# Kernel tuning notes

Hardware: AMD Instinct MI355X
Metric: run time of the kernel (lower is better)

## Reference

```python
import jax, jax.numpy as jnp
import numpy as np

D_MODEL = 1024
N_HEADS = 16
D_Q = 64
D_V = 64
N_SEG = 16
EPS_LN = 1e-5
EPS_MEM = 1e-6


def setup_inputs() -> dict:
    key = jax.random.key(0)
    ks = jax.random.split(key, 10)
    N, T = 4, 4096
    inp = {
        "query_sequences": jax.random.normal(ks[0], (N, T, D_MODEL), dtype=jnp.float32),
        "key_sequences": jax.random.normal(ks[1], (N, T, D_MODEL), dtype=jnp.float32),
        "value_sequences": jax.random.normal(ks[2], (N, T, D_MODEL), dtype=jnp.float32),
        "Wq": jax.random.normal(ks[3], (D_MODEL, N_HEADS * D_Q), dtype=jnp.float32) * 0.02,
        "Wk": jax.random.normal(ks[4], (D_MODEL, N_HEADS * D_Q), dtype=jnp.float32) * 0.02,
        "Wv": jax.random.normal(ks[5], (D_MODEL, N_HEADS * D_V), dtype=jnp.float32) * 0.02,
        "Wo": jax.random.normal(ks[6], (N_HEADS * D_V, D_MODEL), dtype=jnp.float32) * 0.02,
        "ln_w": jnp.ones((D_MODEL,), dtype=jnp.float32),
        "ln_b": jnp.zeros((D_MODEL,), dtype=jnp.float32),
        "beta": jnp.ones((1,), dtype=jnp.float32),
    }
    return inp


def _layer_norm(x, w, b):
    mu = jnp.mean(x, axis=-1, keepdims=True)
    var = jnp.var(x, axis=-1, keepdims=True)
    return (x - mu) * jax.lax.rsqrt(var + EPS_LN) * w + b


def reference(query_sequences, key_sequences, value_sequences, Wq, Wk, Wv, Wo, ln_w, ln_b, beta):
    N, t, _ = query_sequences.shape
    S = t // N_SEG  # segment length (256)

    # qkv_norm applied to q, and (self-attention) to k and v as well
    qn = _layer_norm(query_sequences, ln_w, ln_b)
    kn = _layer_norm(key_sequences, ln_w, ln_b)
    vn = _layer_norm(value_sequences, ln_w, ln_b)

    # project and split heads -> [N, H, t, d]
    qh = (qn @ Wq).reshape(N, t, N_HEADS, D_Q).transpose(0, 2, 1, 3)
    kh = (kn @ Wk).reshape(N, t, N_HEADS, D_Q).transpose(0, 2, 1, 3)
    vh = (vn @ Wv).reshape(N, t, N_HEADS, D_V).transpose(0, 2, 1, 3)

    # segment: [N_SEG, N, H, S, d] so lax.scan iterates segments sequentially
    seg = lambda x, d: x.reshape(N, N_HEADS, N_SEG, S, d).transpose(2, 0, 1, 3, 4)
    q_segs, k_segs, v_segs = seg(qh, D_Q), seg(kh, D_Q), seg(vh, D_V)

    b_gate = jax.nn.sigmoid(beta)[0]            # scalar mixing gate
    scale = 1.0 / np.sqrt(D_Q).astype(np.float32)
    causal = jnp.tril(jnp.ones((S, S), dtype=bool))

    def step(carry, xs):
        mem, z = carry                          # [N,H,Dq,Dv], [N,H,Dq]
        qs, ks_, vs = xs                        # [N,H,S,d]
        sq = jax.nn.elu(qs) + 1.0
        sk = jax.nn.elu(ks_) + 1.0
        # retrieve from compressive memory
        num = jnp.einsum('nhsd,nhde->nhse', sq, mem)
        den = jnp.einsum('nhsd,nhd->nhs', sq, z)[..., None] + EPS_MEM
        a_mem = num / den                       # [N,H,S,Dv]
        # local causal softmax attention within the segment
        scores = jnp.einsum('nhsd,nhtd->nhst', qs, ks_) * scale
        scores = jnp.where(causal, scores, -jnp.inf)
        probs = jax.nn.softmax(scores, axis=-1)
        attn = jnp.einsum('nhst,nhtd->nhsd', probs, vs)
        out = b_gate * a_mem + (1.0 - b_gate) * attn
        # linear memory update
        mem = mem + jnp.einsum('nhsd,nhse->nhde', sk, vs)
        z = z + sk.sum(axis=2)
        return (mem, z), out

    mem0 = jnp.zeros((N, N_HEADS, D_Q, D_V), dtype=query_sequences.dtype)
    z0 = jnp.zeros((N, N_HEADS, D_Q), dtype=query_sequences.dtype)
    _, outs = jax.lax.scan(step, (mem0, z0), (q_segs, k_segs, v_segs))

    # outs: [N_SEG, N, H, S, Dv] -> [N, t, H*Dv]
    seqs = outs.transpose(1, 0, 3, 2, 4).reshape(N, t, N_HEADS * D_V)
    return seqs @ Wo
```

## Files before the change

kernel.cpp:

```cpp
#include <hip/hip_runtime.h>
#include <stdint.h>
#include <math.h>


typedef __attribute__((ext_vector_type(8))) short bf16x8_t;
typedef __attribute__((ext_vector_type(4))) short short4_t;
typedef __attribute__((ext_vector_type(4))) float f32x4;

__device__ __forceinline__ float bf2f(short s){
  union { unsigned u; float f; } v; v.u = ((unsigned)(unsigned short)s) << 16; return v.f;
}
__device__ __forceinline__ short f2bf(float f){
  union { float fl; unsigned u; } v; v.fl = f;
  unsigned r = v.u + 0x7FFFu + ((v.u >> 16) & 1u);
  return (short)(unsigned short)(r >> 16);
}
__device__ __forceinline__ f32x4 mfma16(bf16x8_t a, bf16x8_t b, f32x4 c){
  return __builtin_amdgcn_mfma_f32_16x16x32_bf16(a, b, c, 0, 0, 0);
}
__device__ __forceinline__ void gl_lds16(const short* g, short* l){
  __builtin_amdgcn_global_load_lds((const __attribute__((address_space(1))) void*)g,
                                   (__attribute__((address_space(3))) void*)l, 16, 0, 0);
}

__global__ __launch_bounds__(256) void ln3(const float* __restrict__ xq, const float* __restrict__ xk,
                                           const float* __restrict__ xv,
                                           const float* __restrict__ gw, const float* __restrict__ gb,
                                           short* __restrict__ oq, short* __restrict__ ok,
                                           short* __restrict__ ov){
  const int row = blockIdx.x, which = blockIdx.y, tid = threadIdx.x;
  const float* x = which == 0 ? xq : which == 1 ? xk : xv;
  short* out     = which == 0 ? oq : which == 1 ? ok : ov;
  const float4 v = *reinterpret_cast<const float4*>(x + (size_t)row*1024 + tid*4);
  float s  = v.x + v.y + v.z + v.w;
  float s2 = v.x*v.x + v.y*v.y + v.z*v.z + v.w*v.w;
  #pragma unroll
  for (int off = 1; off < 64; off <<= 1){
    s  += __shfl_xor(s,  off);
    s2 += __shfl_xor(s2, off);
  }
  __shared__ float red[8];
  if ((tid & 63) == 0){ red[tid>>6] = s; red[4 + (tid>>6)] = s2; }
  __syncthreads();
  s  = red[0] + red[1] + red[2] + red[3];
  s2 = red[4] + red[5] + red[6] + red[7];
  const float mu  = s * (1.0f/1024.0f);
  const float var = s2 * (1.0f/1024.0f) - mu*mu;
  const float rs  = rsqrtf(var + 1e-5f);
  const float4 wv = *reinterpret_cast<const float4*>(gw + tid*4);
  const float4 bv = *reinterpret_cast<const float4*>(gb + tid*4);
  short4_t o;
  o[0] = f2bf((v.x-mu)*rs*wv.x + bv.x);
  o[1] = f2bf((v.y-mu)*rs*wv.y + bv.y);
  o[2] = f2bf((v.z-mu)*rs*wv.z + bv.z);
  o[3] = f2bf((v.w-mu)*rs*wv.w + bv.w);
  *reinterpret_cast<short4_t*>(out + (size_t)row*1024 + tid*4) = o;
}

__global__ __launch_bounds__(256) void wcast4(const float* __restrict__ W0, const float* __restrict__ W1,
                                              const float* __restrict__ W2, const float* __restrict__ W3,
                                              short* __restrict__ T0, short* __restrict__ T1,
                                              short* __restrict__ T2, short* __restrict__ T3){
  const int z = blockIdx.z;
  const float* W = z == 0 ? W0 : z == 1 ? W1 : z == 2 ? W2 : W3;
  short* Wt      = z == 0 ? T0 : z == 1 ? T1 : z == 2 ? T2 : T3;
  __shared__ float tile[64][65];
  const int bx = blockIdx.x, by = blockIdx.y, tid = threadIdx.x;
  #pragma unroll
  for (int p=0;p<4;++p){
    int idx = p*256 + tid;
    int r = idx >> 4, c4 = (idx & 15) << 2;
    const float4 v = *reinterpret_cast<const float4*>(W + (size_t)(by*64 + r)*1024 + bx*64 + c4);
    tile[r][c4+0] = v.x; tile[r][c4+1] = v.y; tile[r][c4+2] = v.z; tile[r][c4+3] = v.w;
  }
  __syncthreads();
  #pragma unroll
  for (int p=0;p<4;++p){
    int idx = p*256 + tid;
    int r = idx >> 4, c4 = (idx & 15) << 2;
    short4_t o;
    o[0] = f2bf(tile[c4+0][r]); o[1] = f2bf(tile[c4+1][r]);
    o[2] = f2bf(tile[c4+2][r]); o[3] = f2bf(tile[c4+3][r]);
    *reinterpret_cast<short4_t*>(Wt + (size_t)(bx*64 + r)*1024 + by*64 + c4) = o;
  }
}

__device__ __forceinline__ void remap_mc(int n, int& m0, int& c0){
  int xcd = n & 7, idx = n >> 3;
  m0 = ((xcd << 3) + (idx & 7)) << 8;
  c0 = (idx >> 3) << 8;
}

__device__ __forceinline__ void gemm_body(short* smem, const short* __restrict__ A,
                                          const short* __restrict__ Bt, void* __restrict__ C,
                                          int mode, int m0, int c0){
  short* As = smem;
  short* Bs = smem + 32768;
  const int tid = threadIdx.x;
  const int lane = tid & 63, wid = tid >> 6;
  const int wr = wid >> 2, wc = wid & 3;
  const int l15 = lane & 15, lhi = lane >> 4;

  const short* Asrc[4]; const short* Bsrc[4];
  #pragma unroll
  for (int p=0;p<4;++p){
    int i = tid + 512*p;
    int r = i >> 3, g = (i & 7) ^ (r & 7);
    Asrc[p] = A  + (size_t)(m0 + r)*1024 + g*8;
    Bsrc[p] = Bt + (size_t)(c0 + r)*1024 + g*8;
  }

  f32x4 acc[8][4];
  #pragma unroll
  for (int m=0;m<8;++m)
    #pragma unroll
    for (int n=0;n<4;++n) acc[m][n] = (f32x4){0.f,0.f,0.f,0.f};

  #define STAGE_A(t) { short* _d=&As[((t)&1)<<14]; int _k=(t)<<6; \
      gl_lds16(Asrc[0]+_k, _d+tid*8); gl_lds16(Asrc[1]+_k, _d+4096+tid*8); \
      gl_lds16(Asrc[2]+_k, _d+8192+tid*8); gl_lds16(Asrc[3]+_k, _d+12288+tid*8); }
  #define STAGE_B(t) { short* _d=&Bs[((t)&1)<<14]; int _k=(t)<<6; \
      gl_lds16(Bsrc[0]+_k, _d+tid*8); gl_lds16(Bsrc[1]+_k, _d+4096+tid*8); \
      gl_lds16(Bsrc[2]+_k, _d+8192+tid*8); gl_lds16(Bsrc[3]+_k, _d+12288+tid*8); }

  STAGE_A(0); STAGE_B(0);
  asm volatile("s_waitcnt vmcnt(0)" ::: "memory");
  __builtin_amdgcn_s_barrier();

  for (int t = 0; t < 16; ++t){
    const short* Ab = &As[(t & 1) << 14];
    const short* Bb = &Bs[(t & 1) << 14];
    if (t < 15){ STAGE_A(t+1); STAGE_B(t+1); }
    bf16x8_t af[4][2], bfr[4][2];
    #pragma unroll
    for (int m=0;m<4;++m){
      int r = wr*128 + m*16 + l15;
      #pragma unroll
      for (int ks=0;ks<2;++ks){
        int sl = (ks*4 + lhi) ^ (r & 7);
        af[m][ks] = *reinterpret_cast<const bf16x8_t*>(&Ab[r*64 + sl*8]);
      }
    }
    #pragma unroll
    for (int n=0;n<2;++n){
      int r = wc*64 + n*16 + l15;
      #pragma unroll
      for (int ks=0;ks<2;++ks){
        int sl = (ks*4 + lhi) ^ (r & 7);
        bfr[n][ks] = *reinterpret_cast<const bf16x8_t*>(&Bb[r*64 + sl*8]);
      }
    }
    __builtin_amdgcn_s_setprio(1);
    #pragma unroll
    for (int m=0;m<4;++m)
      #pragma unroll
      for (int n=0;n<2;++n)
        #pragma unroll
        for (int ks=0;ks<2;++ks)
          acc[m][n] = mfma16(af[m][ks], bfr[n][ks], acc[m][n]);
    __builtin_amdgcn_s_setprio(0);
    #pragma unroll
    for (int n=2;n<4;++n){
      int r = wc*64 + n*16 + l15;
      #pragma unroll
      for (int ks=0;ks<2;++ks){
        int sl = (ks*4 + lhi) ^ (r & 7);
        bfr[n][ks] = *reinterpret_cast<const bf16x8_t*>(&Bb[r*64 + sl*8]);
      }
    }
    __builtin_amdgcn_s_setprio(1);
    #pragma unroll
    for (int m=0;m<4;++m)
      #pragma unroll
      for (int n=2;n<4;++n)
        #pragma unroll
        for (int ks=0;ks<2;++ks)
          acc[m][n] = mfma16(af[m][ks], bfr[n][ks], acc[m][n]);
    __builtin_amdgcn_s_setprio(0);
    #pragma unroll
    for (int m=0;m<4;++m){
      int r = wr*128 + 64 + m*16 + l15;
      #pragma unroll
      for (int ks=0;ks<2;++ks){
        int sl = (ks*4 + lhi) ^ (r & 7);
        af[m][ks] = *reinterpret_cast<const bf16x8_t*>(&Ab[r*64 + sl*8]);
      }
    }
    __builtin_amdgcn_s_setprio(1);
    #pragma unroll
    for (int m=0;m<4;++m)
      #pragma unroll
      for (int n=0;n<2;++n)
        #pragma unroll
        for (int ks=0;ks<2;++ks)
          acc[4+m][n] = mfma16(af[m][ks], bfr[n][ks], acc[4+m][n]);
    __builtin_amdgcn_s_setprio(0);
    __builtin_amdgcn_s_setprio(1);
    #pragma unroll
    for (int m=0;m<4;++m)
      #pragma unroll
      for (int n=2;n<4;++n)
        #pragma unroll
        for (int ks=0;ks<2;++ks)
          acc[4+m][n] = mfma16(af[m][ks], bfr[n][ks], acc[4+m][n]);
    __builtin_amdgcn_s_setprio(0);
    asm volatile("s_waitcnt vmcnt(0)" ::: "memory");
    __builtin_amdgcn_s_barrier();
  }
  #undef STAGE_A
  #undef STAGE_B

  if (mode == 0){
    short* Cb = (short*)C;
    #pragma unroll
    for (int m=0;m<8;++m)
      #pragma unroll
      for (int n=0;n<4;++n)
        #pragma unroll
        for (int j=0;j<4;++j){
          int row = m0 + wr*128 + m*16 + lhi*4 + j;
          int col = c0 + wc*64 + n*16 + l15;
          size_t oidx = ((size_t)((row>>12)*16 + (col>>6)) * 4096 + (size_t)(row & 4095)) * 64 + (col & 63);
          Cb[oidx] = f2bf(acc[m][n][j]);
        }
  } else if (mode == 2){
    short* Cb = (short*)C;
    #pragma unroll
    for (int m=0;m<8;++m)
      #pragma unroll
      for (int n=0;n<4;++n){
        int rowb = m0 + wr*128 + m*16 + lhi*4;
        int col  = c0 + wc*64 + n*16 + l15;
        int nh = ((rowb>>12)<<4) + (col>>6);
        int e  = col & 63;
        int tt = rowb & 4095;
        short4_t o;
        #pragma unroll
        for (int j=0;j<4;++j) o[j] = f2bf(acc[m][n][j]);
        *reinterpret_cast<short4_t*>(&Cb[((size_t)nh*64 + e)*4096 + tt]) = o;
      }
  } else {
    float* Cf = (float*)C;
    #pragma unroll
    for (int m=0;m<8;++m)
      #pragma unroll
      for (int n=0;n<4;++n)
        #pragma unroll
        for (int j=0;j<4;++j){
          int row = m0 + wr*128 + m*16 + lhi*4 + j;
          int col = c0 + wc*64 + n*16 + l15;
          Cf[(size_t)row*1024 + col] = acc[m][n][j];
        }
  }
}

__global__ __launch_bounds__(512, 2) void gemm_qkv(const short* __restrict__ A0, const short* __restrict__ A1,
    const short* __restrict__ A2, const short* __restrict__ B0, const short* __restrict__ B1,
    const short* __restrict__ B2, short* __restrict__ C0, short* __restrict__ C1, short* __restrict__ C2){
  extern __shared__ short smem[];
  const int z = blockIdx.z;
  const short* A = z == 0 ? A0 : z == 1 ? A1 : A2;
  const short* B = z == 0 ? B0 : z == 1 ? B1 : B2;
  short* C       = z == 0 ? C0 : z == 1 ? C1 : C2;
  int m0, c0; remap_mc(blockIdx.x + 64*blockIdx.y, m0, c0);
  gemm_body(smem, A, B, (void*)C, z == 2 ? 2 : 0, m0, c0);
}

__global__ __launch_bounds__(512, 2) void gemm_wo(const short* __restrict__ A, const short* __restrict__ Bt,
                                                  float* __restrict__ C){
  extern __shared__ short smem[];
  int m0, c0; remap_mc(blockIdx.x + 64*blockIdx.y, m0, c0);
  gemm_body(smem, A, Bt, (void*)C, 1, m0, c0);
}

__global__ __launch_bounds__(256) void stageA(const short* __restrict__ kh, const short* __restrict__ vhT,
                                              short* __restrict__ delta_b, float* __restrict__ zd){
  const int seg = blockIdx.x, nh = blockIdx.y, tid = threadIdx.x;
  const int lane = tid & 63, w = tid >> 6;
  const int l15 = lane & 15, lhi = lane >> 4;
  __shared__ short skT[64*256];
  const size_t thead = (size_t)nh*4096 + (size_t)seg*256;

  #pragma unroll
  for (int ch=0; ch<8; ++ch){
    int s  = ch*32 + (tid>>3);
    int lc = (tid&7)*8;
    bf16x8_t kv = *reinterpret_cast<const bf16x8_t*>(kh + (thead + s)*64 + lc);
    #pragma unroll
    for (int j=0;j<8;++j){
      float f = bf2f(kv[j]);
      short sv = f2bf((f > 0.f) ? (f + 1.f) : __expf(f));
      int d = lc + j;
      int bo = ((d*256 + s) << 1) ^ (((d>>3)&7) << 4);
      *reinterpret_cast<short*>(reinterpret_cast<char*>(skT) + bo) = sv;
    }
  }
  __syncthreads();

  bf16x8_t ones;
  #pragma unroll
  for (int i=0;i<8;++i) ones[i] = (short)0x3F80;

  f32x4 dacc[4], zacc[4];
  #pragma unroll
  for (int jf=0;jf<4;++jf){ dacc[jf] = (f32x4){0.f,0.f,0.f,0.f}; zacc[jf] = (f32x4){0.f,0.f,0.f,0.f}; }

  #pragma unroll
  for (int ks=0; ks<8; ++ks){
    bf16x8_t av = *reinterpret_cast<const bf16x8_t*>(
        vhT + ((size_t)nh*64 + w*16 + l15)*4096 + (size_t)seg*256 + ks*32 + lhi*8);
    #pragma unroll
    for (int jf=0;jf<4;++jf){
      int d  = jf*16 + l15;
      int so = ks*32 + lhi*8;
      int bo = ((d*256 + so) << 1) ^ (((d>>3)&7) << 4);
      bf16x8_t bk = *reinterpret_cast<const bf16x8_t*>(reinterpret_cast<char*>(skT) + bo);
      dacc[jf] = mfma16(av, bk, dacc[jf]);
      if (w == 0) zacc[jf] = mfma16(ones, bk, zacc[jf]);
    }
  }

  short* dp = delta_b + (size_t)(seg*64 + nh)*4096;
  #pragma unroll
  for (int jf=0;jf<4;++jf)
    #pragma unroll
    for (int j=0;j<4;++j)
      dp[(w*16 + lhi*4 + j)*64 + jf*16 + l15] = f2bf(dacc[jf][j]);
  if (w == 0 && lhi == 0){
    #pragma unroll
    for (int jf=0;jf<4;++jf)
      zd[(size_t)(seg*64 + nh)*64 + jf*16 + l15] = zacc[jf][0];
  }
}

__global__ __launch_bounds__(256) void stageB(const short* __restrict__ delta_b, const float* __restrict__ zd,
                                              short* __restrict__ mpre_b, float* __restrict__ zpre){
  const int c = blockIdx.x, nh = blockIdx.y, tid = threadIdx.x;
  const int idx = c*256 + tid;
  float acc = 0.f;
  for (int seg=0; seg<16; ++seg){
    size_t b = (size_t)(seg*64 + nh)*4096 + idx;
    mpre_b[b] = f2bf(acc);
    acc += bf2f(delta_b[b]);
  }
  if (c == 0 && tid < 64){
    float za = 0.f;
    for (int seg=0; seg<16; ++seg){
      size_t zb = (size_t)(seg*64 + nh)*64 + tid;
      zpre[zb] = za;
      za += zd[zb];
    }
  }
}

__global__ __launch_bounds__(256) void stageC(const short* __restrict__ qh, const short* __restrict__ kh,
    const short* __restrict__ vhT, const short* __restrict__ mpre_b, const float* __restrict__ z_pre,
    const float* __restrict__ beta, short* __restrict__ seqs)
{
  const int seg  = blockIdx.x;
  const int nh   = blockIdx.y;
  const int tid = threadIdx.x;
  const int lane = tid & 63, w = tid >> 6;
  const int l15 = lane & 15, lhi = lane >> 4;

  __shared__ short Ks[2][4096];
  __shared__ short Vs[2][4096];
  __shared__ float zl[64];
  __shared__ short pl[4][64][72];

  const size_t thead = (size_t)nh*4096 + (size_t)seg*256;

  const short* Ksrc[2]; const short* Vsrc[2];
  #pragma unroll
  for (int p=0;p<2;++p){
    int i = tid + 256*p, r = i >> 3, g = (i & 7) ^ (r & 7);
    Ksrc[p] = kh + (thead + r)*64 + g*8;
    Vsrc[p] = vhT + ((size_t)nh*64 + r)*4096 + (size_t)seg*256 + g*8;
  }
  #define STAGE_KV(kt) { short* _kd = Ks[(kt)&1]; short* _vd = Vs[(kt)&1]; \
      gl_lds16(Ksrc[0] + (kt)*4096, _kd + tid*8); \
      gl_lds16(Ksrc[1] + (kt)*4096, _kd + 2048 + tid*8); \
      gl_lds16(Vsrc[0] + (kt)*64,  _vd + tid*8); \
      gl_lds16(Vsrc[1] + (kt)*64,  _vd + 2048 + tid*8); }

  if (tid < 64) zl[tid] = z_pre[(size_t)(seg*64 + nh)*64 + tid];

  bf16x8_t aq[4][2];
  #pragma unroll
  for (int m=0;m<4;++m)
    #pragma unroll
    for (int ks=0;ks<2;++ks)
      aq[m][ks] = *reinterpret_cast<const bf16x8_t*>(qh + (thead + w*64 + m*16 + l15)*64 + ks*32 + lhi*8);

  STAGE_KV(0);
  asm volatile("s_waitcnt vmcnt(0)" ::: "memory");
  __syncthreads();

  const float bg = 1.f / (1.f + __expf(-beta[0]));
  const float scale = 0.125f;
  bf16x8_t ones;
  #pragma unroll
  for (int i=0;i<8;++i) ones[i] = (short)0x3F80;

  f32x4 o_acc[4][4], l_acc[4];
  #pragma unroll
  for (int m=0;m<4;++m){
    l_acc[m] = (f32x4){0.f,0.f,0.f,0.f};
    #pragma unroll
    for (int jf=0;jf<4;++jf) o_acc[m][jf] = (f32x4){0.f,0.f,0.f,0.f};
  }

  for (int kt = 0; kt < 4; ++kt){
    const short* Kb = Ks[kt & 1];
    const short* Vb = Vs[kt & 1];
    if (kt < 3) STAGE_KV(kt+1);
    if (kt <= w){
      f32x4 s_acc[4][4];
      #pragma unroll
      for (int m=0;m<4;++m)
        #pragma unroll
        for (int jf=0;jf<4;++jf) s_acc[m][jf] = (f32x4){0.f,0.f,0.f,0.f};
      #pragma unroll
      for (int ks=0;ks<2;++ks){
        bf16x8_t bk[4];
        #pragma unroll
        for (int jf=0;jf<4;++jf){
          int r = jf*16 + l15;
          int sl = (ks*4 + lhi) ^ (r & 7);
          bk[jf] = *reinterpret_cast<const bf16x8_t*>(&Kb[r*64 + sl*8]);
        }
        #pragma unroll
        for (int m=0;m<4;++m)
          #pragma unroll
          for (int jf=0;jf<4;++jf)
            s_acc[m][jf] = mfma16(aq[m][ks], bk[jf], s_acc[m][jf]);
      }
      const bool diag = (kt == w);
      #pragma unroll
      for (int m=0;m<4;++m)
        #pragma unroll
        for (int jf=0;jf<4;++jf)
          #pragma unroll
          for (int j=0;j<4;++j){
            float vv = s_acc[m][jf][j] * scale;
            if (diag){
              int sr = (w<<6) + m*16 + lhi*4 + j;
              int tc = (kt<<6) + jf*16 + l15;
              if (tc > sr) vv = -INFINITY;
            }
            float pv = __expf(vv);
            pl[w][m*16 + lhi*4 + j][jf*16 + l15] = f2bf(pv);
          }
      #pragma unroll
      for (int ks2=0;ks2<2;++ks2){
        bf16x8_t ap[4], bv[4];
        #pragma unroll
        for (int m=0;m<4;++m)
          ap[m] = *reinterpret_cast<const bf16x8_t*>(&pl[w][m*16 + l15][ks2*32 + lhi*8]);
        #pragma unroll
        for (int jf=0;jf<4;++jf){
          int e = jf*16 + l15;
          int sl = (ks2*4 + lhi) ^ (e & 7);
          bv[jf] = *reinterpret_cast<const bf16x8_t*>(&Vb[e*64 + sl*8]);
        }
        #pragma unroll
        for (int m=0;m<4;++m){
          l_acc[m] = mfma16(ap[m], ones, l_acc[m]);
          #pragma unroll
          for (int jf=0;jf<4;++jf)
            o_acc[m][jf] = mfma16(ap[m], bv[jf], o_acc[m][jf]);
        }
      }
    }
    if (kt < 3){
      asm volatile("s_waitcnt vmcnt(0)" ::: "memory");
      __builtin_amdgcn_s_barrier();
    }
  }
  #undef STAGE_KV

  bf16x8_t sq[4][2];
  #pragma unroll
  for (int m=0;m<4;++m)
    #pragma unroll
    for (int ks=0;ks<2;++ks)
      #pragma unroll
      for (int i=0;i<8;++i){
        float f = bf2f(aq[m][ks][i]);
        sq[m][ks][i] = f2bf((f > 0.f) ? (f + 1.f) : __expf(f));
      }
  bf16x8_t bz[2];
  #pragma unroll
  for (int ks=0;ks<2;++ks)
    #pragma unroll
    for (int i=0;i<8;++i) bz[ks][i] = f2bf(zl[ks*32 + lhi*8 + i]);

  const short* mpbase = mpre_b + (size_t)(seg*64 + nh)*4096;
  f32x4 n_acc[4][4], d_acc[4];
  #pragma unroll
  for (int m=0;m<4;++m){
    d_acc[m] = (f32x4){0.f,0.f,0.f,0.f};
    #pragma unroll
    for (int jf=0;jf<4;++jf) n_acc[m][jf] = (f32x4){0.f,0.f,0.f,0.f};
  }
  #pragma unroll
  for (int ks=0;ks<2;++ks){
    bf16x8_t bm[4];
    #pragma unroll
    for (int jf=0;jf<4;++jf)
      bm[jf] = *reinterpret_cast<const bf16x8_t*>(mpbase + (jf*16 + l15)*64 + ks*32 + lhi*8);
    #pragma unroll
    for (int m=0;m<4;++m){
      #pragma unroll
      for (int jf=0;jf<4;++jf) n_acc[m][jf] = mfma16(sq[m][ks], bm[jf], n_acc[m][jf]);
      d_acc[m] = mfma16(sq[m][ks], bz[ks], d_acc[m]);
    }
  }

  const int nb = nh >> 4, hh = nh & 15;
  #pragma unroll
  for (int m=0;m<4;++m)
    #pragma unroll
    for (int jf=0;jf<4;++jf)
      #pragma unroll
      for (int j=0;j<4;++j){
        float attn = o_acc[m][jf][j] / l_acc[m][j];
        float amem = n_acc[m][jf][j] / (d_acc[m][j] + 1e-6f);
        float ov = bg*amem + (1.f-bg)*attn;
        int srow = (w<<6) + m*16 + lhi*4 + j;
        seqs[((size_t)nb*4096 + (size_t)seg*256 + srow)*1024 + hh*64 + jf*16 + l15] = f2bf(ov);
      }
}

extern "C" void kernel_launch(void* const* d_in, const int* in_sizes, int n_in,
                              void* d_out, int out_size, void* d_ws, size_t ws_size,
                              hipStream_t stream){
  (void)in_sizes; (void)n_in; (void)out_size; (void)ws_size;
  const float* q    = (const float*)d_in[0];
  const float* k    = (const float*)d_in[1];
  const float* v    = (const float*)d_in[2];
  const float* Wq   = (const float*)d_in[3];
  const float* Wk   = (const float*)d_in[4];
  const float* Wv   = (const float*)d_in[5];
  const float* Wo   = (const float*)d_in[6];
  const float* lnw  = (const float*)d_in[7];
  const float* lnb  = (const float*)d_in[8];
  const float* beta = (const float*)d_in[9];
  char* ws = (char*)d_ws;
  const size_t MB = 1024ull*1024ull;
  short* WqT    = (short*)(ws + 0*MB);
  short* WkT    = (short*)(ws + 2*MB);
  short* WvT    = (short*)(ws + 4*MB);
  short* WoT    = (short*)(ws + 6*MB);
  short* xn_v   = (short*)(ws + 8*MB);
  short* seqs   = xn_v;
  short* qh     = (short*)(ws + 40*MB);
  short* kh     = (short*)(ws + 72*MB);
  short* vhT    = (short*)(ws + 104*MB);
  short* delta_b= (short*)(ws + 136*MB);
  float* zd     = (float*)(ws + 144*MB);
  short* mpre_b = (short*)(ws + 145*MB);
  float* zpre   = (float*)(ws + 153*MB);
  short* xn_q   = (short*)d_out;
  short* xn_k   = (short*)d_out + 16384ull*1024ull;

  wcast4<<<dim3(16,16,4),256,0,stream>>>(Wq,Wk,Wv,Wo, WqT,WkT,WvT,WoT);
  ln3<<<dim3(16384,3),256,0,stream>>>(q,k,v, lnw,lnb, xn_q,xn_k,xn_v);

  const size_t lds_gemm = 131072;
  gemm_qkv<<<dim3(64,4,3),512,lds_gemm,stream>>>(xn_q,xn_k,xn_v, WqT,WkT,WvT, qh,kh,vhT);

  stageA<<<dim3(16,64),256,0,stream>>>(kh, vhT, delta_b, zd);
  stageB<<<dim3(16,64),256,0,stream>>>(delta_b, zd, mpre_b, zpre);
  stageC<<<dim3(16,64),256,0,stream>>>(qh, kh, vhT, mpre_b, zpre, beta, seqs);
  gemm_wo<<<dim3(64,4),512,lds_gemm,stream>>>(seqs, WoT, (float*)d_out);
}
```

Before: 310.4 us.

## Split GEMM tile loads into half-stages interleaved with MFMA phases

Result: no change. 307.9 us (-0.8%).

```diff
diff --git a/kernel.cpp b/kernel.cpp
--- a/kernel.cpp
+++ b/kernel.cpp
@@ -116,21 +116,23 @@
     #pragma unroll
     for (int n=0;n<4;++n) acc[m][n] = (f32x4){0.f,0.f,0.f,0.f};
 
-  #define STAGE_A(t) { short* _d=&As[((t)&1)<<14]; int _k=(t)<<6; \
-      gl_lds16(Asrc[0]+_k, _d+tid*8); gl_lds16(Asrc[1]+_k, _d+4096+tid*8); \
+  #define STAGE_A0(t) { short* _d=&As[((t)&1)<<14]; int _k=(t)<<6; \
+      gl_lds16(Asrc[0]+_k, _d+tid*8); gl_lds16(Asrc[1]+_k, _d+4096+tid*8); }
+  #define STAGE_A1(t) { short* _d=&As[((t)&1)<<14]; int _k=(t)<<6; \
       gl_lds16(Asrc[2]+_k, _d+8192+tid*8); gl_lds16(Asrc[3]+_k, _d+12288+tid*8); }
-  #define STAGE_B(t) { short* _d=&Bs[((t)&1)<<14]; int _k=(t)<<6; \
-      gl_lds16(Bsrc[0]+_k, _d+tid*8); gl_lds16(Bsrc[1]+_k, _d+4096+tid*8); \
+  #define STAGE_B0(t) { short* _d=&Bs[((t)&1)<<14]; int _k=(t)<<6; \
+      gl_lds16(Bsrc[0]+_k, _d+tid*8); gl_lds16(Bsrc[1]+_k, _d+4096+tid*8); }
+  #define STAGE_B1(t) { short* _d=&Bs[((t)&1)<<14]; int _k=(t)<<6; \
       gl_lds16(Bsrc[2]+_k, _d+8192+tid*8); gl_lds16(Bsrc[3]+_k, _d+12288+tid*8); }
 
-  STAGE_A(0); STAGE_B(0);
-  asm volatile("s_waitcnt vmcnt(0)" ::: "memory");
+  STAGE_B0(0); STAGE_A0(0); STAGE_B1(0); STAGE_A1(0);
+  STAGE_B0(1); STAGE_A0(1);
+  asm volatile("s_waitcnt vmcnt(4)" ::: "memory");
   __builtin_amdgcn_s_barrier();
 
   for (int t = 0; t < 16; ++t){
     const short* Ab = &As[(t & 1) << 14];
     const short* Bb = &Bs[(t & 1) << 14];
-    if (t < 15){ STAGE_A(t+1); STAGE_B(t+1); }
     bf16x8_t af[4][2], bfr[4][2];
     #pragma unroll
     for (int m=0;m<4;++m){
@@ -150,6 +152,7 @@
         bfr[n][ks] = *reinterpret_cast<const bf16x8_t*>(&Bb[r*64 + sl*8]);
       }
     }
+    if (t < 15) STAGE_B1(t+1);
     __builtin_amdgcn_s_setprio(1);
     #pragma unroll
     for (int m=0;m<4;++m)
@@ -168,6 +171,7 @@
         bfr[n][ks] = *reinterpret_cast<const bf16x8_t*>(&Bb[r*64 + sl*8]);
       }
     }
+    if (t < 15) STAGE_A1(t+1);
     __builtin_amdgcn_s_setprio(1);
     #pragma unroll
     for (int m=0;m<4;++m)
@@ -177,6 +181,9 @@
         for (int ks=0;ks<2;++ks)
           acc[m][n] = mfma16(af[m][ks], bfr[n][ks], acc[m][n]);
     __builtin_amdgcn_s_setprio(0);
+    asm volatile("" ::: "memory");
+    __builtin_amdgcn_s_barrier();
+    asm volatile("" ::: "memory");
     #pragma unroll
     for (int m=0;m<4;++m){
       int r = wr*128 + 64 + m*16 + l15;
@@ -186,6 +193,7 @@
         af[m][ks] = *reinterpret_cast<const bf16x8_t*>(&Ab[r*64 + sl*8]);
       }
     }
+    if (t < 14) STAGE_B0(t+2);
     __builtin_amdgcn_s_setprio(1);
     #pragma unroll
     for (int m=0;m<4;++m)
@@ -195,6 +203,10 @@
         for (int ks=0;ks<2;++ks)
           acc[4+m][n] = mfma16(af[m][ks], bfr[n][ks], acc[4+m][n]);
     __builtin_amdgcn_s_setprio(0);
+    asm volatile("" ::: "memory");
+    __builtin_amdgcn_s_barrier();
+    asm volatile("" ::: "memory");
+    if (t < 14) STAGE_A0(t+2);
     __builtin_amdgcn_s_setprio(1);
     #pragma unroll
     for (int m=0;m<4;++m)
@@ -204,11 +216,14 @@
         for (int ks=0;ks<2;++ks)
           acc[4+m][n] = mfma16(af[m][ks], bfr[n][ks], acc[4+m][n]);
     __builtin_amdgcn_s_setprio(0);
-    asm volatile("s_waitcnt vmcnt(0)" ::: "memory");
-    __builtin_amdgcn_s_barrier();
-  }
-  #undef STAGE_A
-  #undef STAGE_B
+    if (t < 14)       { asm volatile("s_waitcnt vmcnt(4)" ::: "memory"); }
+    else if (t == 14) { asm volatile("s_waitcnt vmcnt(0)" ::: "memory"); }
+    if (t < 15) __builtin_amdgcn_s_barrier();
+  }
+  #undef STAGE_A0
+  #undef STAGE_A1
+  #undef STAGE_B0
+  #undef STAGE_B1
 
   if (mode == 0){
     short* Cb = (short*)C;
```
